# Optimization experiments

Measured on AMD Instinct MI355X. Metric: run time of the kernel, lower is better.

The kernel has to match this reference:

```python
import jax, jax.numpy as jnp
import numpy as np

HEADS = 16

def setup_inputs() -> dict:
    key = jax.random.key(0)
    k0, k1, k2, k3 = jax.random.split(key, 4)
    B, L, D = 2, 2048, 2048
    q = jax.random.normal(k0, (B, L, D), dtype=jnp.float32)
    k = jax.random.normal(k1, (B, L, D), dtype=jnp.float32)
    v = jax.random.normal(k2, (B, L, D), dtype=jnp.float32)
    wo = jax.random.normal(k3, (D, D), dtype=jnp.float32) * (1.0 / np.sqrt(D))
    return {"q": q, "k": k, "v": v, "wo": wo}

def reference(q, k, v, wo):
    B, Lq, D = q.shape
    Lk = k.shape[1]
    H = HEADS
    hd = D // H
    # [B, L, D] -> [B, H, L, hd]
    qh = q.reshape(B, Lq, H, hd).transpose(0, 2, 1, 3)
    kh = k.reshape(B, Lk, H, hd).transpose(0, 2, 1, 3)
    vh = v.reshape(B, Lk, H, hd).transpose(0, 2, 1, 3)
    scale = 1.0 / np.sqrt(hd).astype(np.float32)
    scores = jnp.einsum('bhqd,bhkd->bhqk', qh, kh) * scale
    cache_len = Lk - Lq
    # additive causal mask: -10000 above diagonal offset cache_len+1
    mask = jnp.triu(jnp.full((Lq, Lk), -10000.0, dtype=scores.dtype), k=cache_len + 1)
    attn = jax.nn.softmax(scores + mask, axis=-1)  # dropout p=0.0 => identity
    out = jnp.einsum('bhqk,bhkd->bhqd', attn, vh)
    out = out.transpose(0, 2, 1, 3).reshape(B, Lq, D)
    out = out @ wo.T  # torch Linear: x @ W^T
    return (out, kh, vh)
```

## Files before the change

### kernel.cpp

```cpp
#include <hip/hip_runtime.h>


typedef __attribute__((ext_vector_type(8))) __bf16 bf16x8;
typedef __attribute__((ext_vector_type(4))) __bf16 bf16x4;
typedef __attribute__((ext_vector_type(4))) float f32x4;

__device__ __forceinline__ unsigned short f2bf(float f) {
  union { float f; unsigned int u; } v; v.f = f;
  return (unsigned short)((v.u + 0x7FFFu + ((v.u >> 16) & 1u)) >> 16);
}
__device__ __forceinline__ f32x4 zero4() {
  f32x4 z = {0.0f, 0.0f, 0.0f, 0.0f};
  return z;
}
__device__ __forceinline__ void gld_lds16(const unsigned short* g, unsigned short* l) {
  __builtin_amdgcn_global_load_lds(
      (const __attribute__((address_space(1))) unsigned int*)g,
      (__attribute__((address_space(3))) unsigned int*)l, 16, 0, 0);
}

__global__ __launch_bounds__(256) void conv_k(const float* __restrict__ k,
                                              float* __restrict__ kh,
                                              unsigned short* __restrict__ kbf) {
  int t = blockIdx.x * 256 + threadIdx.x;
  int d4 = t & 31;
  int l  = (t >> 5) & 2047;
  int h  = (t >> 16) & 15;
  int b  = t >> 20;
  const float4 v = *(const float4*)(k + ((size_t)(b * 2048 + l)) * 2048 + h * 128 + d4 * 4);
  size_t dst = (size_t)t * 4;
  *(float4*)(kh + dst) = v;
  *(ushort4*)(kbf + dst) = make_ushort4(f2bf(v.x), f2bf(v.y), f2bf(v.z), f2bf(v.w));
}

__global__ __launch_bounds__(256) void conv_wo(const float* __restrict__ wo,
                                               unsigned short* __restrict__ wobf) {
  int t = blockIdx.x * 256 + threadIdx.x;
  size_t dst = (size_t)t * 4;
  const float4 v = *(const float4*)(wo + dst);
  *(ushort4*)(wobf + dst) = make_ushort4(f2bf(v.x), f2bf(v.y), f2bf(v.z), f2bf(v.w));
}

__global__ __launch_bounds__(256) void conv_v(const float* __restrict__ v,
                                              float* __restrict__ vh,
                                              unsigned short* __restrict__ vbt) {
  __shared__ __align__(16) unsigned short T[128 * 72];
  const int tid = threadIdx.x;
  const int bid = blockIdx.x;
  const int lt = bid & 31;
  const int h  = (bid >> 5) & 15;
  const int b  = bid >> 9;
  const int l0 = lt * 64;
  const int bh = b * 16 + h;
#pragma unroll
  for (int i = 0; i < 8; ++i) {
    int c = tid + 256 * i;
    int row = c >> 5, col4 = c & 31;
    const float4 x = *(const float4*)(v + ((size_t)(b * 2048 + l0 + row)) * 2048 + h * 128 + col4 * 4);
    *(float4*)(vh + ((size_t)(bh * 2048 + l0 + row)) * 128 + col4 * 4) = x;
    T[(col4 * 4 + 0) * 72 + row] = f2bf(x.x);
    T[(col4 * 4 + 1) * 72 + row] = f2bf(x.y);
    T[(col4 * 4 + 2) * 72 + row] = f2bf(x.z);
    T[(col4 * 4 + 3) * 72 + row] = f2bf(x.w);
  }
  __syncthreads();
#pragma unroll
  for (int i = 0; i < 4; ++i) {
    int c = tid + 256 * i;
    int dR = c >> 3, cIdx = c & 7;
    int s2 = cIdx >> 2, qd = cIdx & 3;
    const unsigned short* Tr = &T[dR * 72];
    uint4 o4;
    o4.x = *(const unsigned int*)&Tr[0 * 16 + qd * 4 + 2 * s2];
    o4.y = *(const unsigned int*)&Tr[1 * 16 + qd * 4 + 2 * s2];
    o4.z = *(const unsigned int*)&Tr[2 * 16 + qd * 4 + 2 * s2];
    o4.w = *(const unsigned int*)&Tr[3 * 16 + qd * 4 + 2 * s2];
    *(uint4*)(vbt + ((size_t)(bh * 128 + dR)) * 2048 + l0 + cIdx * 8) = o4;
  }
}

__global__ __launch_bounds__(512) void flash_attn(const float* __restrict__ q,
                                                  const unsigned short* __restrict__ kbf,
                                                  const unsigned short* __restrict__ vbt,
                                                  unsigned short* __restrict__ ctx) {
  __shared__ __align__(16) unsigned short K3[3][64 * 128];
  __shared__ __align__(16) unsigned short V3[3][128 * 64];
  const int tid = threadIdx.x;
  const int w = tid >> 6, lane = tid & 63;
  const int lo = lane & 15, quad = lane >> 4;
  const int bid = blockIdx.x;
  const int pair = bid & 7;
  const int bh = bid >> 3;
  const int b = bh >> 4, h = bh & 15;
  const unsigned short* kg0 = kbf + (size_t)bh * 2048 * 128;
  const unsigned short* vg0 = vbt + (size_t)bh * 128 * 2048;
  const float qscale = 0.08838834764831845f * 1.4426950408889634f;

  auto stage = [&](int buf, int k0) {
#pragma unroll
    for (int i = 0; i < 2; ++i) {
      int c = tid + 512 * i;
      int row = c >> 4, p = c & 15;
      int g = (p & 8) | ((p & 7) ^ (row & 7));
      gld_lds16(kg0 + (size_t)(k0 + row) * 128 + g * 8, &K3[buf][(w * 64 + 512 * i) * 8]);
    }
#pragma unroll
    for (int i = 0; i < 2; ++i) {
      int c = tid + 512 * i;
      int row = c >> 3, p = c & 7;
      int g = p ^ (row & 7);
      gld_lds16(vg0 + (size_t)row * 2048 + k0 + g * 8, &V3[buf][(w * 64 + 512 * i) * 8]);
    }
  };

  for (int phase = 0; phase < 2; ++phase) {
    const int qt = phase ? 15 - pair : pair;
    const int q0 = qt * 128;
    const int qrow = q0 + w * 16 + lo;
    const int ktlim = 2 * qt + 2;

    bf16x8 qf[4];
    {
      const float* qb = q + ((size_t)(b * 2048 + q0 + w * 16 + lo)) * 2048 + h * 128;
#pragma unroll
      for (int kb = 0; kb < 4; ++kb) {
        float4 x = *(const float4*)(qb + kb * 32 + quad * 8);
        float4 y = *(const float4*)(qb + kb * 32 + quad * 8 + 4);
        bf16x8 f;
        f[0] = (__bf16)(x.x * qscale); f[1] = (__bf16)(x.y * qscale);
        f[2] = (__bf16)(x.z * qscale); f[3] = (__bf16)(x.w * qscale);
        f[4] = (__bf16)(y.x * qscale); f[5] = (__bf16)(y.y * qscale);
        f[6] = (__bf16)(y.z * qscale); f[7] = (__bf16)(y.w * qscale);
        qf[kb] = f;
      }
    }

    stage(0, 0);
    asm volatile("" ::: "memory");
    stage(1, 64);
    asm volatile("" ::: "memory");

    f32x4 o[8];
#pragma unroll
    for (int i = 0; i < 8; ++i) o[i] = zero4();
    float lsum = 0.0f;

    for (int kt = 0; kt < ktlim; ++kt) {
      if (kt + 1 < ktlim) {
        asm volatile("s_waitcnt vmcnt(4)" ::: "memory");
      } else {
        asm volatile("s_waitcnt vmcnt(0)" ::: "memory");
      }
      __builtin_amdgcn_s_barrier();
      if (kt + 2 < ktlim) {
        stage((kt + 2) % 3, (kt + 2) * 64);
        asm volatile("" ::: "memory");
      }
      const int buf = kt % 3;
      const int k0 = kt * 64;

      if (k0 <= q0 + w * 16 + 15) {
        f32x4 s[4];
#pragma unroll
        for (int nb = 0; nb < 4; ++nb) {
          f32x4 z = zero4();
#pragma unroll
          for (int kb = 0; kb < 4; ++kb) {
            int row = nb * 16 + lo;
            int g = kb * 4 + quad;
            int p = (g & 8) | ((g & 7) ^ (row & 7));
            bf16x8 kf = *(const bf16x8*)&K3[buf][row * 128 + p * 8];
            z = __builtin_amdgcn_mfma_f32_16x16x32_bf16(kf, qf[kb], z, 0, 0, 0);
          }
          s[nb] = z;
        }

        if (kt >= 2 * qt) {
#pragma unroll
          for (int nb = 0; nb < 4; ++nb) {
            int keyb = k0 + nb * 16 + quad * 4;
#pragma unroll
            for (int r = 0; r < 4; ++r) {
              if (keyb + r > qrow) s[nb][r] = -1e30f;
            }
          }
        }

        bf16x8 pa[2];
#pragma unroll
        for (int nb = 0; nb < 4; ++nb) {
#pragma unroll
          for (int s2 = 0; s2 < 2; ++s2) {
            float p0 = __builtin_amdgcn_exp2f(s[nb][2 * s2]);
            float p1 = __builtin_amdgcn_exp2f(s[nb][2 * s2 + 1]);
            lsum += p0 + p1;
            pa[s2][2 * nb]     = (__bf16)p0;
            pa[s2][2 * nb + 1] = (__bf16)p1;
          }
        }

#pragma unroll
        for (int ob = 0; ob < 8; ++ob) {
#pragma unroll
          for (int kb2 = 0; kb2 < 2; ++kb2) {
            int row = ob * 16 + lo;
            int g = kb2 * 4 + quad;
            int p = g ^ (row & 7);
            bf16x8 vf = *(const bf16x8*)&V3[buf][row * 64 + p * 8];
            o[ob] = __builtin_amdgcn_mfma_f32_16x16x32_bf16(vf, pa[kb2], o[ob], 0, 0, 0);
          }
        }
      }
    }
    __syncthreads();

    lsum += __shfl_xor(lsum, 16);
    lsum += __shfl_xor(lsum, 32);
    const float linv = 1.0f / lsum;

    unsigned short* cb = ctx + ((size_t)(b * 2048 + q0 + w * 16 + lo)) * 2048 + h * 128 + quad * 4;
#pragma unroll
    for (int ob = 0; ob < 8; ++ob) {
      bf16x4 pk4;
      pk4[0] = (__bf16)(o[ob][0] * linv);
      pk4[1] = (__bf16)(o[ob][1] * linv);
      pk4[2] = (__bf16)(o[ob][2] * linv);
      pk4[3] = (__bf16)(o[ob][3] * linv);
      *(bf16x4*)(cb + ob * 16) = pk4;
    }
  }
}

__global__ __launch_bounds__(256) void gemm_bt(const unsigned short* __restrict__ A,
                                               const unsigned short* __restrict__ Bm,
                                               float* __restrict__ C) {
  __shared__ __align__(16) unsigned short As[2][128 * 64];
  __shared__ __align__(16) unsigned short Bs[2][128 * 64];
  const int tid = threadIdx.x;
  const int w = tid >> 6, lane = tid & 63;
  const int lo = lane & 15, quad = lane >> 4;
  const int nbid = blockIdx.x & 15;
  const int mbid = blockIdx.x >> 4;
  const int m0 = mbid * 128, n0 = nbid * 128;
  const int wr = w >> 1, wc = w & 1;

  auto stage = [&](int buf, int k0) {
#pragma unroll
    for (int i = 0; i < 4; ++i) {
      int c = tid + 256 * i;
      int row = c >> 3, p = c & 7;
      int g = p ^ (row & 7);
      gld_lds16(A + (size_t)(m0 + row) * 2048 + k0 + g * 8, &As[buf][(w * 64 + 256 * i) * 8]);
    }
#pragma unroll
    for (int i = 0; i < 4; ++i) {
      int c = tid + 256 * i;
      int row = c >> 3, p = c & 7;
      int g = p ^ (row & 7);
      gld_lds16(Bm + (size_t)(n0 + row) * 2048 + k0 + g * 8, &Bs[buf][(w * 64 + 256 * i) * 8]);
    }
  };

  f32x4 acc[4][4];
#pragma unroll
  for (int i = 0; i < 4; ++i)
#pragma unroll
    for (int j = 0; j < 4; ++j) acc[i][j] = zero4();

  stage(0, 0);
  for (int kt = 0; kt < 32; ++kt) {
    __syncthreads();
    if (kt < 31) stage((kt + 1) & 1, (kt + 1) * 64);
    const int buf = kt & 1;
#pragma unroll
    for (int kb = 0; kb < 2; ++kb) {
      bf16x8 af[4], bfr[4];
#pragma unroll
      for (int mi = 0; mi < 4; ++mi) {
        int row = wr * 64 + mi * 16 + lo;
        int g = kb * 4 + quad;
        int p = g ^ (row & 7);
        af[mi] = *(const bf16x8*)&As[buf][row * 64 + p * 8];
      }
#pragma unroll
      for (int ni = 0; ni < 4; ++ni) {
        int row = wc * 64 + ni * 16 + lo;
        int g = kb * 4 + quad;
        int p = g ^ (row & 7);
        bfr[ni] = *(const bf16x8*)&Bs[buf][row * 64 + p * 8];
      }
#pragma unroll
      for (int mi = 0; mi < 4; ++mi)
#pragma unroll
        for (int ni = 0; ni < 4; ++ni)
          acc[mi][ni] = __builtin_amdgcn_mfma_f32_16x16x32_bf16(af[mi], bfr[ni], acc[mi][ni], 0, 0, 0);
    }
  }
#pragma unroll
  for (int mi = 0; mi < 4; ++mi)
#pragma unroll
    for (int ni = 0; ni < 4; ++ni)
#pragma unroll
      for (int r = 0; r < 4; ++r) {
        int row = m0 + wr * 64 + mi * 16 + quad * 4 + r;
        int col = n0 + wc * 64 + ni * 16 + lo;
        C[(size_t)row * 2048 + col] = acc[mi][ni][r];
      }
}

extern "C" void kernel_launch(void* const* d_in, const int* in_sizes, int n_in,
                              void* d_out, int out_size, void* d_ws, size_t ws_size,
                              hipStream_t stream) {
  const float* q  = (const float*)d_in[0];
  const float* k  = (const float*)d_in[1];
  const float* v  = (const float*)d_in[2];
  const float* wo = (const float*)d_in[3];

  float* outp = (float*)d_out;
  float* kh   = outp + 8388608;
  float* vh   = outp + 16777216;

  unsigned short* ws   = (unsigned short*)d_ws;
  unsigned short* kbf  = ws;
  unsigned short* vbt  = kbf + 8388608;
  unsigned short* wobf = vbt + 8388608;
  unsigned short* ctx  = wobf + 4194304;

  conv_k<<<8192, 256, 0, stream>>>(k, kh, kbf);
  conv_v<<<1024, 256, 0, stream>>>(v, vh, vbt);
  conv_wo<<<4096, 256, 0, stream>>>(wo, wobf);
  flash_attn<<<256, 512, 0, stream>>>(q, kbf, vbt, ctx);
  gemm_bt<<<512, 256, 0, stream>>>(ctx, wobf, outp);
}
```

Measured before the change: 297.5 us.

## Split key tile across warp pairs with 32-row query tiles and LDS reduction

```diff
diff --git a/kernel.cpp b/kernel.cpp
--- a/kernel.cpp
+++ b/kernel.cpp
@@ -68,13 +68,14 @@
   for (int i = 0; i < 4; ++i) {
     int c = tid + 256 * i;
     int dR = c >> 3, cIdx = c & 7;
-    int s2 = cIdx >> 2, qd = cIdx & 3;
+    int kh2 = cIdx >> 2, qd = cIdx & 3;
     const unsigned short* Tr = &T[dR * 72];
+    int base = kh2 * 32 + qd * 4;
     uint4 o4;
-    o4.x = *(const unsigned int*)&Tr[0 * 16 + qd * 4 + 2 * s2];
-    o4.y = *(const unsigned int*)&Tr[1 * 16 + qd * 4 + 2 * s2];
-    o4.z = *(const unsigned int*)&Tr[2 * 16 + qd * 4 + 2 * s2];
-    o4.w = *(const unsigned int*)&Tr[3 * 16 + qd * 4 + 2 * s2];
+    o4.x = *(const unsigned int*)&Tr[base + 0];
+    o4.y = *(const unsigned int*)&Tr[base + 2];
+    o4.z = *(const unsigned int*)&Tr[base + 16];
+    o4.w = *(const unsigned int*)&Tr[base + 18];
     *(uint4*)(vbt + ((size_t)(bh * 128 + dR)) * 2048 + l0 + cIdx * 8) = o4;
   }
 }
@@ -83,11 +84,13 @@
                                                   const unsigned short* __restrict__ kbf,
                                                   const unsigned short* __restrict__ vbt,
                                                   unsigned short* __restrict__ ctx) {
-  __shared__ __align__(16) unsigned short K3[3][64 * 128];
-  __shared__ __align__(16) unsigned short V3[3][128 * 64];
+  __shared__ __align__(16) unsigned char smem[98304];
+  unsigned short* K3 = (unsigned short*)smem;
+  unsigned short* V3 = (unsigned short*)(smem + 49152);
   const int tid = threadIdx.x;
   const int w = tid >> 6, lane = tid & 63;
   const int lo = lane & 15, quad = lane >> 4;
+  const int rg = w & 3, kh2 = w >> 2;
   const int bid = blockIdx.x;
   const int pair = bid & 7;
   const int bh = bid >> 3;
@@ -97,31 +100,34 @@
   const float qscale = 0.08838834764831845f * 1.4426950408889634f;
 
   auto stage = [&](int buf, int k0) {
+    unsigned short* Kb = K3 + buf * 8192;
+    unsigned short* Vb = V3 + buf * 8192;
 #pragma unroll
     for (int i = 0; i < 2; ++i) {
       int c = tid + 512 * i;
       int row = c >> 4, p = c & 15;
       int g = (p & 8) | ((p & 7) ^ (row & 7));
-      gld_lds16(kg0 + (size_t)(k0 + row) * 128 + g * 8, &K3[buf][(w * 64 + 512 * i) * 8]);
+      gld_lds16(kg0 + (size_t)(k0 + row) * 128 + g * 8, Kb + (w * 64 + 512 * i) * 8);
     }
 #pragma unroll
     for (int i = 0; i < 2; ++i) {
       int c = tid + 512 * i;
       int row = c >> 3, p = c & 7;
       int g = p ^ (row & 7);
-      gld_lds16(vg0 + (size_t)row * 2048 + k0 + g * 8, &V3[buf][(w * 64 + 512 * i) * 8]);
+      gld_lds16(vg0 + (size_t)row * 2048 + k0 + g * 8, Vb + (w * 64 + 512 * i) * 8);
     }
   };
 
   for (int phase = 0; phase < 2; ++phase) {
     const int qt = phase ? 15 - pair : pair;
     const int q0 = qt * 128;
-    const int qrow = q0 + w * 16 + lo;
     const int ktlim = 2 * qt + 2;
-
-    bf16x8 qf[4];
-    {
-      const float* qb = q + ((size_t)(b * 2048 + q0 + w * 16 + lo)) * 2048 + h * 128;
+    const int rowmax = q0 + rg * 32 + 31;
+
+    bf16x8 qf[2][4];
+#pragma unroll
+    for (int s = 0; s < 2; ++s) {
+      const float* qb = q + ((size_t)(b * 2048 + q0 + rg * 32 + s * 16 + lo)) * 2048 + h * 128;
 #pragma unroll
       for (int kb = 0; kb < 4; ++kb) {
         float4 x = *(const float4*)(qb + kb * 32 + quad * 8);
@@ -131,7 +137,7 @@
         f[2] = (__bf16)(x.z * qscale); f[3] = (__bf16)(x.w * qscale);
         f[4] = (__bf16)(y.x * qscale); f[5] = (__bf16)(y.y * qscale);
         f[6] = (__bf16)(y.z * qscale); f[7] = (__bf16)(y.w * qscale);
-        qf[kb] = f;
+        qf[s][kb] = f;
       }
     }
 
@@ -140,10 +146,12 @@
     stage(1, 64);
     asm volatile("" ::: "memory");
 
-    f32x4 o[8];
-#pragma unroll
-    for (int i = 0; i < 8; ++i) o[i] = zero4();
-    float lsum = 0.0f;
+    f32x4 o[2][8];
+#pragma unroll
+    for (int s = 0; s < 2; ++s)
+#pragma unroll
+      for (int i = 0; i < 8; ++i) o[s][i] = zero4();
+    float lsum[2] = {0.0f, 0.0f};
 
     for (int kt = 0; kt < ktlim; ++kt) {
       if (kt + 1 < ktlim) {
@@ -156,78 +164,115 @@
         stage((kt + 2) % 3, (kt + 2) * 64);
         asm volatile("" ::: "memory");
       }
-      const int buf = kt % 3;
+      const unsigned short* Kb = K3 + (kt % 3) * 8192;
+      const unsigned short* Vb = V3 + (kt % 3) * 8192;
       const int k0 = kt * 64;
-
-      if (k0 <= q0 + w * 16 + 15) {
-        f32x4 s[4];
-#pragma unroll
-        for (int nb = 0; nb < 4; ++nb) {
-          f32x4 z = zero4();
+      const int kbase = k0 + kh2 * 32;
+
+      if (kbase <= rowmax) {
+        f32x4 sv[2][2];
+#pragma unroll
+        for (int nb = 0; nb < 2; ++nb) {
+          bf16x8 kf[4];
+          int row = kh2 * 32 + nb * 16 + lo;
 #pragma unroll
           for (int kb = 0; kb < 4; ++kb) {
-            int row = nb * 16 + lo;
             int g = kb * 4 + quad;
             int p = (g & 8) | ((g & 7) ^ (row & 7));
-            bf16x8 kf = *(const bf16x8*)&K3[buf][row * 128 + p * 8];
-            z = __builtin_amdgcn_mfma_f32_16x16x32_bf16(kf, qf[kb], z, 0, 0, 0);
+            kf[kb] = *(const bf16x8*)(Kb + row * 128 + p * 8);
           }
-          s[nb] = z;
+#pragma unroll
+          for (int s = 0; s < 2; ++s) {
+            f32x4 z = zero4();
+#pragma unroll
+            for (int kb = 0; kb < 4; ++kb)
+              z = __builtin_amdgcn_mfma_f32_16x16x32_bf16(kf[kb], qf[s][kb], z, 0, 0, 0);
+            sv[s][nb] = z;
+          }
         }
 
         if (kt >= 2 * qt) {
 #pragma unroll
-          for (int nb = 0; nb < 4; ++nb) {
-            int keyb = k0 + nb * 16 + quad * 4;
-#pragma unroll
-            for (int r = 0; r < 4; ++r) {
-              if (keyb + r > qrow) s[nb][r] = -1e30f;
+          for (int s = 0; s < 2; ++s) {
+            int qrow = q0 + rg * 32 + s * 16 + lo;
+#pragma unroll
+            for (int nb = 0; nb < 2; ++nb) {
+              int keyb = kbase + nb * 16 + quad * 4;
+#pragma unroll
+              for (int r = 0; r < 4; ++r) {
+                if (keyb + r > qrow) sv[s][nb][r] = -1e30f;
+              }
             }
           }
         }
 
         bf16x8 pa[2];
 #pragma unroll
-        for (int nb = 0; nb < 4; ++nb) {
-#pragma unroll
-          for (int s2 = 0; s2 < 2; ++s2) {
-            float p0 = __builtin_amdgcn_exp2f(s[nb][2 * s2]);
-            float p1 = __builtin_amdgcn_exp2f(s[nb][2 * s2 + 1]);
-            lsum += p0 + p1;
-            pa[s2][2 * nb]     = (__bf16)p0;
-            pa[s2][2 * nb + 1] = (__bf16)p1;
-          }
+        for (int s = 0; s < 2; ++s) {
+          bf16x8 f;
+#pragma unroll
+          for (int nb = 0; nb < 2; ++nb)
+#pragma unroll
+            for (int t2 = 0; t2 < 2; ++t2) {
+              float p0 = __builtin_amdgcn_exp2f(sv[s][nb][2 * t2]);
+              float p1 = __builtin_amdgcn_exp2f(sv[s][nb][2 * t2 + 1]);
+              lsum[s] += p0 + p1;
+              f[(nb * 2 + t2) * 2]     = (__bf16)p0;
+              f[(nb * 2 + t2) * 2 + 1] = (__bf16)p1;
+            }
+          pa[s] = f;
         }
 
 #pragma unroll
         for (int ob = 0; ob < 8; ++ob) {
-#pragma unroll
-          for (int kb2 = 0; kb2 < 2; ++kb2) {
-            int row = ob * 16 + lo;
-            int g = kb2 * 4 + quad;
-            int p = g ^ (row & 7);
-            bf16x8 vf = *(const bf16x8*)&V3[buf][row * 64 + p * 8];
-            o[ob] = __builtin_amdgcn_mfma_f32_16x16x32_bf16(vf, pa[kb2], o[ob], 0, 0, 0);
-          }
+          int row = ob * 16 + lo;
+          int g = kh2 * 4 + quad;
+          int p = g ^ (row & 7);
+          bf16x8 vf = *(const bf16x8*)(Vb + row * 64 + p * 8);
+#pragma unroll
+          for (int s = 0; s < 2; ++s)
+            o[s][ob] = __builtin_amdgcn_mfma_f32_16x16x32_bf16(vf, pa[s], o[s][ob], 0, 0, 0);
         }
       }
     }
     __syncthreads();
 
-    lsum += __shfl_xor(lsum, 16);
-    lsum += __shfl_xor(lsum, 32);
-    const float linv = 1.0f / lsum;
-
-    unsigned short* cb = ctx + ((size_t)(b * 2048 + q0 + w * 16 + lo)) * 2048 + h * 128 + quad * 4;
-#pragma unroll
-    for (int ob = 0; ob < 8; ++ob) {
-      bf16x4 pk4;
-      pk4[0] = (__bf16)(o[ob][0] * linv);
-      pk4[1] = (__bf16)(o[ob][1] * linv);
-      pk4[2] = (__bf16)(o[ob][2] * linv);
-      pk4[3] = (__bf16)(o[ob][3] * linv);
-      *(bf16x4*)(cb + ob * 16) = pk4;
-    }
+#pragma unroll
+    for (int s = 0; s < 2; ++s) {
+      lsum[s] += __shfl_xor(lsum[s], 16);
+      lsum[s] += __shfl_xor(lsum[s], 32);
+    }
+
+    float* ored = (float*)smem;
+    float* lred = ored + 16384;
+    if (kh2 == 1) {
+#pragma unroll
+      for (int s = 0; s < 2; ++s)
+#pragma unroll
+        for (int ob = 0; ob < 8; ++ob)
+          *(f32x4*)(ored + (((rg * 16 + s * 8 + ob) * 64 + lane) << 2)) = o[s][ob];
+      lred[(rg * 64 + lane) * 2 + 0] = lsum[0];
+      lred[(rg * 64 + lane) * 2 + 1] = lsum[1];
+    }
+    __syncthreads();
+    if (kh2 == 0) {
+#pragma unroll
+      for (int s = 0; s < 2; ++s) {
+        const float li = 1.0f / (lsum[s] + lred[(rg * 64 + lane) * 2 + s]);
+        unsigned short* cb = ctx + ((size_t)(b * 2048 + q0 + rg * 32 + s * 16 + lo)) * 2048 + h * 128 + quad * 4;
+#pragma unroll
+        for (int ob = 0; ob < 8; ++ob) {
+          const f32x4 po = *(const f32x4*)(ored + (((rg * 16 + s * 8 + ob) * 64 + lane) << 2));
+          bf16x4 pk4;
+          pk4[0] = (__bf16)((o[s][ob][0] + po[0]) * li);
+          pk4[1] = (__bf16)((o[s][ob][1] + po[1]) * li);
+          pk4[2] = (__bf16)((o[s][ob][2] + po[2]) * li);
+          pk4[3] = (__bf16)((o[s][ob][3] + po[3]) * li);
+          *(bf16x4*)(cb + ob * 16) = pk4;
+        }
+      }
+    }
+    __syncthreads();
   }
 }
 
```

New measurement: 290.5 us. 2.4% less time.
